# Optimization experiments

Hardware: AMD Instinct MI355X
Metric: run time of the kernel (lower is better)

## Reference

```python
import jax, jax.numpy as jnp
import numpy as np

N, E, B, D, OUT = 15000, 60000, 512, 64, 12
NI, EI, EH = 15, 5, 128
STEPS = 6  # both num_step_message_passing and num_step_set2set


def setup_inputs():
    key = jax.random.key(0)
    ks = jax.random.split(key, 30)
    r = lambda k, s, sc=0.05: jax.random.normal(k, s, jnp.float32) * sc
    return {
        "x": r(ks[0], (N, NI), 1.0),
        "edge_attr": r(ks[1], (E, EI), 1.0),
        "edge_index": jax.random.randint(ks[2], (2, E), 0, N),
        "batch": jnp.sort(jax.random.randint(ks[3], (N,), 0, B)),
        "lin0_w": r(ks[4], (D, NI)), "lin0_b": r(ks[5], (D,)),
        "en_w1": r(ks[6], (EH, EI)), "en_b1": r(ks[7], (EH,)),
        "en_w2": r(ks[8], (D * D, EH)), "en_b2": r(ks[9], (D * D,)),
        "conv_b": r(ks[10], (D,)),
        "gru_w_ih": r(ks[11], (3 * D, D)), "gru_w_hh": r(ks[12], (3 * D, D)),
        "gru_b_ih": r(ks[13], (3 * D,)), "gru_b_hh": r(ks[14], (3 * D,)),
        "lstm_w_ih": r(ks[15], (4 * D, 2 * D)), "lstm_w_hh": r(ks[16], (4 * D, D)),
        "lstm_b_ih": r(ks[17], (4 * D,)), "lstm_b_hh": r(ks[18], (4 * D,)),
        "lin1_w": r(ks[19], (D, 2 * D)), "lin1_b": r(ks[20], (D,)),
        "lin2_w": r(ks[21], (OUT, D)), "lin2_b": r(ks[22], (OUT,)),
    }


def _forward(x, edge_attr, lin0_w, lin0_b, en_w1, en_b1, en_w2, en_b2, conv_b,
             gru_w_ih, gru_w_hh, gru_b_ih, gru_b_hh,
             lstm_w_ih, lstm_w_hh, lstm_b_ih, lstm_b_hh,
             lin1_w, lin1_b, lin2_w, lin2_b, edge_index, batch):
    src, tgt = edge_index[0], edge_index[1]
    deg = jnp.maximum(jax.ops.segment_sum(jnp.ones((E,), x.dtype), tgt, num_segments=N), 1.0)
    # NNConv edge network (edge_attr is constant across MP steps -> hoist; same math)
    ew = jax.nn.relu(edge_attr @ en_w1.T + en_b1) @ en_w2.T + en_b2
    ew = ew.reshape(E, D, D)  # [E, in, out] per-edge weight matrices

    out = jax.nn.relu(x @ lin0_w.T + lin0_b)  # lin0
    h = out  # GRU hidden state (num_layers=1, seq_len=1)
    for _ in range(STEPS):
        # gather -> per-edge matvec -> scatter-mean (NNConv, aggr='mean', root_weight=False)
        msg = jnp.einsum('ei,eio->eo', out[src], ew)
        agg = jax.ops.segment_sum(msg, tgt, num_segments=N) / deg[:, None]
        m = jax.nn.relu(agg + conv_b)
        # single GRU step (PyTorch gate layout: r, z, n)
        gi = m @ gru_w_ih.T + gru_b_ih
        gh = h @ gru_w_hh.T + gru_b_hh
        ir, iz, inn = jnp.split(gi, 3, axis=-1)
        hr, hz, hn = jnp.split(gh, 3, axis=-1)
        rg = jax.nn.sigmoid(ir + hr)
        zg = jax.nn.sigmoid(iz + hz)
        ng = jnp.tanh(inn + rg * hn)
        h = (1.0 - zg) * ng + zg * h
        out = h

    # Set2Set pooling (LSTM gate layout: i, f, g, o)
    q_star = jnp.zeros((B, 2 * D), x.dtype)
    hl = jnp.zeros((B, D), x.dtype)
    cl = jnp.zeros((B, D), x.dtype)
    for _ in range(STEPS):
        g = q_star @ lstm_w_ih.T + lstm_b_ih + hl @ lstm_w_hh.T + lstm_b_hh
        ig, fg, gg, og = jnp.split(g, 4, axis=-1)
        cl = jax.nn.sigmoid(fg) * cl + jax.nn.sigmoid(ig) * jnp.tanh(gg)
        hl = jax.nn.sigmoid(og) * jnp.tanh(cl)
        e = jnp.sum(out * hl[batch], axis=-1)  # [N] attention logits
        emax = jax.ops.segment_max(e, batch, num_segments=B)
        ex = jnp.exp(e - emax[batch])
        denom = jax.ops.segment_sum(ex, batch, num_segments=B)
        a = ex / (denom[batch] + 1e-16)  # batch-segmented softmax
        rvec = jax.ops.segment_sum(a[:, None] * out, batch, num_segments=B)
        q_star = jnp.concatenate([hl, rvec], axis=-1)

    y = jax.nn.relu(q_star @ lin1_w.T + lin1_b) @ lin2_w.T + lin2_b
    return y  # [B, OUT]


def reference(x, edge_attr, edge_index, batch, lin0_w, lin0_b, en_w1, en_b1, en_w2, en_b2,
              conv_b, gru_w_ih, gru_w_hh, gru_b_ih, gru_b_hh,
              lstm_w_ih, lstm_w_hh, lstm_b_ih, lstm_b_hh, lin1_w, lin1_b, lin2_w, lin2_b):
    return _forward(x, edge_attr, lin0_w, lin0_b, en_w1, en_b1, en_w2, en_b2, conv_b,
                    gru_w_ih, gru_w_hh, gru_b_ih, gru_b_hh,
                    lstm_w_ih, lstm_w_hh, lstm_b_ih, lstm_b_hh,
                    lin1_w, lin1_b, lin2_w, lin2_b, edge_index, batch)
```

## Files before the change

kernel.cpp:

```cpp
#include <hip/hip_runtime.h>
#include <hip/hip_bf16.h>
#include <math.h>

#define NN 15000
#define NE 60000
#define NB 512
#define NIF 15
#define EIF 5
#define EHID 128
#define NSTEP 6
#define EPB 128

typedef _Float16 half8 __attribute__((ext_vector_type(8)));
typedef float floatx4 __attribute__((ext_vector_type(4)));

typedef __attribute__((address_space(3))) _Float16 lds_f16;
typedef __attribute__((address_space(1))) const _Float16 glb_f16;

__device__ __forceinline__ void gload_lds16(const _Float16* g, _Float16* l) {
  __builtin_amdgcn_global_load_lds((glb_f16*)g, (lds_f16*)l, 16, 0, 0);
}

__device__ __forceinline__ float sigmoidf_(float x) { return 1.f / (1.f + expf(-x)); }

__global__ void k_sentinel(float* out) { out[0] = 1000.0f; }

__global__ void k_init(const float* __restrict__ x, const float* __restrict__ l0w,
                       const float* __restrict__ l0b, const int* __restrict__ tgt,
                       const int* __restrict__ batch, float* __restrict__ outv,
                       float* __restrict__ deg, int* __restrict__ gstart,
                       int* __restrict__ gend,
                       const float* __restrict__ ea, const float* __restrict__ w1,
                       const float* __restrict__ b1,
                       const float* __restrict__ w2, const float* __restrict__ b2,
                       const float* __restrict__ gwih, const float* __restrict__ gwhh,
                       const float* __restrict__ lwih, const float* __restrict__ lwhh,
                       _Float16* __restrict__ w2pp, _Float16* __restrict__ hidp,
                       _Float16* __restrict__ wgpk,
                       float* __restrict__ wTih, float* __restrict__ wThh) {
  int idx = blockIdx.x * 256 + threadIdx.x;
  if (idx < NN * 64) {
    int n = idx >> 6, d = idx & 63;
    float s = l0b[d];
#pragma unroll
    for (int i = 0; i < NIF; ++i) s += x[n * NIF + i] * l0w[d * NIF + i];
    outv[idx] = fmaxf(s, 0.f);
  }
  if (idx < NE) atomicAdd(&deg[tgt[idx]], 1.0f);
  if (idx < NN) {
    int bb = batch[idx];
    atomicMin(&gstart[bb], idx);
    atomicMax(&gend[bb], idx + 1);
  }
  {
    int ih = idx - NN * 64;
    if (ih >= 0 && ih < NE * 16) {
      int e = ih >> 4, part = ih & 15;
      float eav[EIF];
#pragma unroll
      for (int i = 0; i < EIF; ++i) eav[i] = ea[e * EIF + i];
      half8 hv;
#pragma unroll
      for (int j = 0; j < 8; ++j) {
        int h = part * 8 + j;
        float s = b1[h];
#pragma unroll
        for (int i = 0; i < EIF; ++i) s += eav[i] * w1[h * EIF + i];
        hv[j] = (_Float16)fmaxf(s, 0.f);
      }
      *(half8*)&hidp[(size_t)e * 128 + part * 8] = hv;
    }
  }
  if (idx < 528384) {
    int g = idx >> 9;
    int r = idx & 511;
    int o = r >> 3, j = r & 7;
    float v;
    if (g < 1024) {
      int i = g >> 4;
      int h = ((g & 15) << 3) + j;
      v = w2[(size_t)(i * 64 + o) * 128 + h];
    } else {
      int i = ((g - 1024) << 3) + j;
      v = b2[i * 64 + o];
    }
    w2pp[idx] = (_Float16)v;
  } else if (idx < 528384 + 24576) {
    int i2 = idx - 528384;
    int kc = i2 / 6144;
    int rem = i2 % 6144;
    int o = rem >> 5, r = rem & 31;
    int kind = kc >> 1, cc = kc & 1;
    float v = kind ? gwhh[o * 64 + cc * 32 + r] : gwih[o * 64 + cc * 32 + r];
    wgpk[i2] = (_Float16)v;
  } else if (idx < 528384 + 24576 + 32768) {
    int i3 = idx - (528384 + 24576);
    int k = i3 >> 8, g = i3 & 255;
    wTih[i3] = lwih[g * 128 + k];
  } else if (idx < 528384 + 24576 + 32768 + 16384) {
    int i4 = idx - (528384 + 24576 + 32768);
    int k = i4 >> 8, g = i4 & 255;
    wThh[i4] = lwhh[g * 64 + k];
  }
}

__global__ __launch_bounds__(256, 4) void k_msg(
    const float* __restrict__ outv, const _Float16* __restrict__ hidp,
    const _Float16* __restrict__ w2pp, const int* __restrict__ src,
    const int* __restrict__ tgt, float* __restrict__ agg) {
  __shared__ __align__(16) _Float16 osL[EPB][72];
  __shared__ __align__(16) _Float16 bS[2][4096];
  int tid = threadIdx.x;
  int e0 = blockIdx.x * EPB;
  int hb = blockIdx.y;
  const int cbase = hb * 2;

  int el = tid >> 1, hf = tid & 1;
  int e = e0 + el;
  bool valid = e < NE;
  int s = valid ? src[e] : 0;
  const float4* op = (const float4*)(outv + (size_t)s * 64 + hf * 32);
#pragma unroll
  for (int pr = 0; pr < 4; ++pr) {
    float4 va = op[pr * 2 + 0];
    float4 vb = op[pr * 2 + 1];
    if (!valid) { va = vb = make_float4(0.f, 0.f, 0.f, 0.f); }
    half8 pk;
    pk[0] = (_Float16)va.x; pk[1] = (_Float16)va.y;
    pk[2] = (_Float16)va.z; pk[3] = (_Float16)va.w;
    pk[4] = (_Float16)vb.x; pk[5] = (_Float16)vb.y;
    pk[6] = (_Float16)vb.z; pk[7] = (_Float16)vb.w;
    *(half8*)&osL[el][hf * 32 + pr * 8] = pk;
  }

  int wv = tid >> 6, lane = tid & 63;
  int l15 = lane & 15, q = lane >> 4;
  int rbase = wv * 32 + l15;

  half8 hidf[2][2];
#pragma unroll
  for (int m = 0; m < 2; ++m) {
    int ef = e0 + rbase + m * 16;
    if (ef > NE - 1) ef = NE - 1;
    const _Float16* hp = hidp + (size_t)ef * 128 + hb * 64 + q * 8;
    hidf[m][0] = *(const half8*)hp;
    hidf[m][1] = *(const half8*)(hp + 32);
  }

  __syncthreads();

  {
    const _Float16* g0 = w2pp + (size_t)cbase * 2048 + tid * 8;
    gload_lds16(g0, &bS[0][0] + tid * 8);
    gload_lds16(g0 + 2048, &bS[0][0] + tid * 8 + 2048);
    const _Float16* g1 = w2pp + (size_t)(cbase + 4) * 2048 + tid * 8;
    gload_lds16(g1, &bS[1][0] + tid * 8);
    gload_lds16(g1 + 2048, &bS[1][0] + tid * 8 + 2048);
  }

  floatx4 acc[2][4];
#pragma unroll
  for (int m = 0; m < 2; ++m)
#pragma unroll
    for (int og = 0; og < 4; ++og) acc[m][og] = (floatx4){0.f, 0.f, 0.f, 0.f};

  const int fbase = q * 512 + l15 * 8;

  for (int il = 0; il < 64; ++il) {
    int p = il & 1;
    _Float16 osv0 = osL[rbase][il];
    _Float16 osv1 = osL[rbase + 16][il];
    if (il < 63) {
      asm volatile("s_waitcnt vmcnt(2)" ::: "memory");
    } else {
      asm volatile("s_waitcnt vmcnt(0)" ::: "memory");
    }
    __builtin_amdgcn_s_barrier();
    half8 fr[2][4];
    const _Float16* bb = &bS[p][0];
#pragma unroll
    for (int hc = 0; hc < 2; ++hc)
#pragma unroll
      for (int og = 0; og < 4; ++og)
        fr[hc][og] = *(const half8*)&bb[hc * 2048 + fbase + og * 128];
    asm volatile("s_waitcnt lgkmcnt(0)" ::: "memory");
    __builtin_amdgcn_sched_barrier(0);
    __builtin_amdgcn_s_barrier();
    if (il < 62) {
      const _Float16* gsrc = w2pp + (size_t)(cbase + (il + 2) * 4) * 2048 + tid * 8;
      _Float16* ldst = &bS[p][0] + tid * 8;
      gload_lds16(gsrc, ldst);
      gload_lds16(gsrc + 2048, ldst + 2048);
    }
    half8 os0 = {osv0, osv0, osv0, osv0, osv0, osv0, osv0, osv0};
    half8 os1 = {osv1, osv1, osv1, osv1, osv1, osv1, osv1, osv1};
#pragma unroll
    for (int hc = 0; hc < 2; ++hc) {
      half8 af0 = hidf[0][hc] * os0;
      half8 af1 = hidf[1][hc] * os1;
#pragma unroll
      for (int og = 0; og < 4; ++og) {
        acc[0][og] = __builtin_amdgcn_mfma_f32_16x16x32_f16(af0, fr[hc][og], acc[0][og], 0, 0, 0);
        acc[1][og] = __builtin_amdgcn_mfma_f32_16x16x32_f16(af1, fr[hc][og], acc[1][og], 0, 0, 0);
      }
    }
  }

  if (hb == 0) {
#pragma unroll
    for (int ibb = 0; ibb < 2; ++ibb) {
      int cb = 256 + ibb;
      const _Float16* bp = w2pp + ((size_t)(cb * 4 + q) * 64 + l15) * 8;
      half8 af[2];
#pragma unroll
      for (int m = 0; m < 2; ++m)
        af[m] = *(const half8*)&osL[rbase + m * 16][ibb * 32 + q * 8];
#pragma unroll
      for (int og = 0; og < 4; ++og) {
        half8 bf = *(const half8*)(bp + og * 128);
#pragma unroll
        for (int m = 0; m < 2; ++m)
          acc[m][og] = __builtin_amdgcn_mfma_f32_16x16x32_f16(af[m], bf, acc[m][og], 0, 0, 0);
      }
    }
  }

#pragma unroll
  for (int m = 0; m < 2; ++m) {
    int erow = e0 + wv * 32 + m * 16 + q * 4;
#pragma unroll
    for (int j = 0; j < 4; ++j) {
      int ee = erow + j;
      if (ee < NE) {
        int t = tgt[ee];
        float* ap = agg + (size_t)t * 64 + l15;
#pragma unroll
        for (int og = 0; og < 4; ++og) atomicAdd(ap + og * 16, acc[m][og][j]);
      }
    }
  }
}

__global__ __launch_bounds__(128, 2) void k_gru(
    float* __restrict__ agg, const float* __restrict__ deg,
    const float* __restrict__ convb, const _Float16* __restrict__ wgpk,
    const float* __restrict__ bih, const float* __restrict__ bhh,
    float* __restrict__ outv) {
  __shared__ __align__(16) _Float16 aL[32][136];
  __shared__ float hF[32][68];
  __shared__ float cbL[64];
  int tid = threadIdx.x;
  int n0 = blockIdx.x * 32;
  if (tid < 64) cbL[tid] = convb[tid];
  __syncthreads();

  int nl = tid >> 2, dq = (tid & 3) * 16;
  int n = n0 + nl;
  if (n < NN) {
    float dg = fmaxf(deg[n], 1.f);
    const float4* ap = (const float4*)(agg + (size_t)n * 64 + dq);
    const float4* hp = (const float4*)(outv + (size_t)n * 64 + dq);
    float4* az = (float4*)(agg + (size_t)n * 64 + dq);
#pragma unroll
    for (int t = 0; t < 4; ++t) {
      float4 a = ap[t];
      float4 h = hp[t];
      int d = dq + t * 4;
      aL[nl][d + 0] = (_Float16)fmaxf(a.x / dg + cbL[d + 0], 0.f);
      aL[nl][d + 1] = (_Float16)fmaxf(a.y / dg + cbL[d + 1], 0.f);
      aL[nl][d + 2] = (_Float16)fmaxf(a.z / dg + cbL[d + 2], 0.f);
      aL[nl][d + 3] = (_Float16)fmaxf(a.w / dg + cbL[d + 3], 0.f);
      aL[nl][64 + d + 0] = (_Float16)h.x;
      aL[nl][64 + d + 1] = (_Float16)h.y;
      aL[nl][64 + d + 2] = (_Float16)h.z;
      aL[nl][64 + d + 3] = (_Float16)h.w;
      hF[nl][d + 0] = h.x; hF[nl][d + 1] = h.y;
      hF[nl][d + 2] = h.z; hF[nl][d + 3] = h.w;
      az[t] = make_float4(0.f, 0.f, 0.f, 0.f);
    }
  } else {
#pragma unroll
    for (int t = 0; t < 4; ++t) {
      int d = dq + t * 4;
#pragma unroll
      for (int u = 0; u < 4; ++u) {
        aL[nl][d + u] = (_Float16)0.f;
        aL[nl][64 + d + u] = (_Float16)0.f;
        hF[nl][d + u] = 0.f;
      }
    }
  }
  __syncthreads();

  int wv = tid >> 6, lane = tid & 63, l15 = lane & 15, qd = lane >> 4;
  floatx4 acc[2][6][2];
#pragma unroll
  for (int mt = 0; mt < 2; ++mt)
#pragma unroll
    for (int t6 = 0; t6 < 6; ++t6)
#pragma unroll
      for (int kind = 0; kind < 2; ++kind) acc[mt][t6][kind] = (floatx4){0.f, 0.f, 0.f, 0.f};

#pragma unroll
  for (int kind = 0; kind < 2; ++kind) {
#pragma unroll
    for (int cc = 0; cc < 2; ++cc) {
      half8 af[2];
#pragma unroll
      for (int mt = 0; mt < 2; ++mt)
        af[mt] = *(const half8*)&aL[mt * 16 + l15][kind * 64 + cc * 32 + qd * 8];
#pragma unroll
      for (int t6 = 0; t6 < 6; ++t6) {
        int gb = (t6 * 2 + wv) * 16;
        half8 bf = *(const half8*)&wgpk[((size_t)(kind * 2 + cc) * 192 + gb + l15) * 32 + qd * 8];
#pragma unroll
        for (int mt = 0; mt < 2; ++mt)
          acc[mt][t6][kind] = __builtin_amdgcn_mfma_f32_16x16x32_f16(af[mt], bf, acc[mt][t6][kind], 0, 0, 0);
      }
    }
  }

#pragma unroll
  for (int dd = 0; dd < 2; ++dd) {
    int d = (dd * 2 + wv) * 16 + l15;
    float bir = bih[d], bhr = bhh[d];
    float biz = bih[64 + d], bhz = bhh[64 + d];
    float bin = bih[128 + d], bhn = bhh[128 + d];
#pragma unroll
    for (int mt = 0; mt < 2; ++mt) {
#pragma unroll
      for (int j = 0; j < 4; ++j) {
        int nloc = mt * 16 + qd * 4 + j;
        int nn = n0 + nloc;
        if (nn < NN) {
          float ir = acc[mt][dd][0][j] + bir, hr = acc[mt][dd][1][j] + bhr;
          float iz = acc[mt][2 + dd][0][j] + biz, hz = acc[mt][2 + dd][1][j] + bhz;
          float in_ = acc[mt][4 + dd][0][j] + bin, hn = acc[mt][4 + dd][1][j] + bhn;
          float r = sigmoidf_(ir + hr);
          float z = sigmoidf_(iz + hz);
          float ng = tanhf(in_ + r * hn);
          float h = hF[nloc][d];
          outv[(size_t)nn * 64 + d] = (1.f - z) * ng + z * h;
        }
      }
    }
  }
}

__global__ __launch_bounds__(256) void k_s2s(
    const float* __restrict__ outv, const int* __restrict__ gstart,
    const int* __restrict__ gend, const float* __restrict__ wTih,
    const float* __restrict__ wThh, const float* __restrict__ bih,
    const float* __restrict__ bhh, const float* __restrict__ l1w,
    const float* __restrict__ l1b, const float* __restrict__ l2w,
    const float* __restrict__ l2b, float* __restrict__ y) {
  __shared__ float qL[128], hlL[64], clL[64], gL[256];
  __shared__ float mxA[4], smA[4], accA[4][64], hidL[64];
  int b = blockIdx.x, tid = threadIdx.x, wv = tid >> 6, lane = tid & 63;
  int s0 = gstart[b], e0 = gend[b];
  if (s0 > e0) { s0 = 0; e0 = 0; }
  if (tid < 128) qL[tid] = 0.f;
  if (tid < 64) { hlL[tid] = 0.f; clL[tid] = 0.f; }
  __syncthreads();

  for (int step = 0; step < NSTEP; ++step) {
    {
      int g = tid;
      float s = bih[g] + bhh[g];
      for (int k = 0; k < 128; ++k) s += qL[k] * wTih[k * 256 + g];
      for (int k = 0; k < 64; ++k) s += hlL[k] * wThh[k * 256 + g];
      gL[g] = s;
    }
    __syncthreads();
    if (tid < 64) {
      float ig = gL[tid], fg = gL[64 + tid], gg = gL[128 + tid], og = gL[192 + tid];
      float c = sigmoidf_(fg) * clL[tid] + sigmoidf_(ig) * tanhf(gg);
      clL[tid] = c;
      hlL[tid] = sigmoidf_(og) * tanhf(c);
    }
    __syncthreads();
    float hd = hlL[lane];
    float mxw = -1e30f;
    for (int nn = s0 + wv; nn < e0; nn += 4) {
      float v = outv[(size_t)nn * 64 + lane] * hd;
#pragma unroll
      for (int off = 32; off > 0; off >>= 1) v += __shfl_xor(v, off);
      mxw = fmaxf(mxw, v);
    }
    if (lane == 0) mxA[wv] = mxw;
    __syncthreads();
    float mx = fmaxf(fmaxf(mxA[0], mxA[1]), fmaxf(mxA[2], mxA[3]));
    float sm = 0.f, ac = 0.f;
    for (int nn = s0 + wv; nn < e0; nn += 4) {
      float o_nd = outv[(size_t)nn * 64 + lane];
      float v = o_nd * hd;
#pragma unroll
      for (int off = 32; off > 0; off >>= 1) v += __shfl_xor(v, off);
      float ex = expf(v - mx);
      sm += ex;
      ac += ex * o_nd;
    }
    if (lane == 0) smA[wv] = sm;
    accA[wv][lane] = ac;
    __syncthreads();
    if (tid < 64) {
      float den = smA[0] + smA[1] + smA[2] + smA[3] + 1e-16f;
      float rv = (accA[0][tid] + accA[1][tid] + accA[2][tid] + accA[3][tid]) / den;
      qL[tid] = hlL[tid];
      qL[64 + tid] = rv;
    }
    __syncthreads();
  }
  if (tid < 64) {
    float s = l1b[tid];
    for (int k = 0; k < 128; ++k) s += qL[k] * l1w[tid * 128 + k];
    hidL[tid] = fmaxf(s, 0.f);
  }
  __syncthreads();
  if (tid < 12) {
    float s = l2b[tid];
    for (int k = 0; k < 64; ++k) s += hidL[k] * l2w[tid * 64 + k];
    y[b * 12 + tid] = s;
  }
}

extern "C" void kernel_launch(void* const* d_in, const int* in_sizes, int n_in,
                              void* d_out, int out_size, void* d_ws, size_t ws_size,
                              hipStream_t stream) {
  const float* x = (const float*)d_in[0];
  const float* ea = (const float*)d_in[1];
  const int* eidx = (const int*)d_in[2];
  const int* batch = (const int*)d_in[3];
  const float* lin0_w = (const float*)d_in[4];
  const float* lin0_b = (const float*)d_in[5];
  const float* en_w1 = (const float*)d_in[6];
  const float* en_b1 = (const float*)d_in[7];
  const float* en_w2 = (const float*)d_in[8];
  const float* en_b2 = (const float*)d_in[9];
  const float* conv_b = (const float*)d_in[10];
  const float* gru_wih = (const float*)d_in[11];
  const float* gru_whh = (const float*)d_in[12];
  const float* gru_bih = (const float*)d_in[13];
  const float* gru_bhh = (const float*)d_in[14];
  const float* lstm_wih = (const float*)d_in[15];
  const float* lstm_whh = (const float*)d_in[16];
  const float* lstm_bih = (const float*)d_in[17];
  const float* lstm_bhh = (const float*)d_in[18];
  const float* lin1_w = (const float*)d_in[19];
  const float* lin1_b = (const float*)d_in[20];
  const float* lin2_w = (const float*)d_in[21];
  const float* lin2_b = (const float*)d_in[22];
  const int* srcp = eidx;
  const int* tgtp = eidx + NE;

  char* ws = (char*)d_ws;
  size_t off = 0;
  auto alloc = [&](size_t bytes) {
    char* p = ws + off;
    off += (bytes + 255) & ~(size_t)255;
    return p;
  };
  _Float16* w2pp = (_Float16*)alloc((size_t)1032 * 512 * 2);
  _Float16* hidp = (_Float16*)alloc((size_t)NE * 128 * 2);
  _Float16* wgpk = (_Float16*)alloc((size_t)24576 * 2);
  float* wTih = (float*)alloc((size_t)32768 * 4);
  float* wThh = (float*)alloc((size_t)16384 * 4);
  float* out = (float*)alloc((size_t)NN * 64 * 4);
  float* agg = (float*)alloc((size_t)NN * 64 * 4);
  float* deg = (float*)alloc((size_t)NN * 4);
  int* gstart = (int*)alloc((size_t)NB * 4);
  int* gend = (int*)alloc((size_t)NB * 4);
  if (off > ws_size) {
    k_sentinel<<<1, 1, 0, stream>>>((float*)d_out);
    return;
  }

  hipMemsetAsync(deg, 0, (size_t)NN * 4, stream);
  hipMemsetAsync(gstart, 0x7f, (size_t)NB * 4, stream);
  hipMemsetAsync(gend, 0, (size_t)NB * 4, stream);
  hipMemsetAsync(agg, 0, (size_t)NN * 64 * 4, stream);

  k_init<<<(NN * 64 + NE * 16 + 255) / 256, 256, 0, stream>>>(
      x, lin0_w, lin0_b, tgtp, batch, out, deg, gstart, gend,
      ea, en_w1, en_b1, en_w2, en_b2, gru_wih, gru_whh, lstm_wih, lstm_whh,
      w2pp, hidp, wgpk, wTih, wThh);

  for (int step = 0; step < NSTEP; ++step) {
    k_msg<<<dim3((NE + EPB - 1) / EPB, 2), 256, 0, stream>>>(out, hidp, w2pp,
                                                             srcp, tgtp, agg);
    k_gru<<<(NN + 31) / 32, 128, 0, stream>>>(agg, deg, conv_b, wgpk, gru_bih,
                                              gru_bhh, out);
  }

  k_s2s<<<NB, 256, 0, stream>>>(out, gstart, gend, wTih, wThh, lstm_bih, lstm_bhh,
                                lin1_w, lin1_b, lin2_w, lin2_b, (float*)d_out);
}
```

Baseline: 692.8 us.

## Split message kernel across output halves instead of hidden halves

The second grid dimension of the per-edge message kernel now splits the 64 output columns into two halves instead of splitting the 128-wide hidden dimension. Each block accumulates over all 128 hidden units for its 32 outputs. Partial sums over hidden units no longer have to be combined through atomics, so each edge issues half as many atomicAdds per block and the total atomic count drops. In exchange, each block loads twice as many hidden fragments into registers, and the weight tiles are fetched with a strided remapped layout that may be less coalesced.

After: 674.4 us. -2.7%, faster.

```diff
diff --git a/kernel.cpp b/kernel.cpp
--- a/kernel.cpp
+++ b/kernel.cpp
@@ -112,8 +112,13 @@
   __shared__ __align__(16) _Float16 bS[2][4096];
   int tid = threadIdx.x;
   int e0 = blockIdx.x * EPB;
-  int hb = blockIdx.y;
-  const int cbase = hb * 2;
+  int oh = blockIdx.y;
+
+  const int hcA = tid >> 7, qA = (tid >> 5) & 3, opA = tid & 31;
+  const size_t srcA = (size_t)qA * 512 + oh * 256 + opA * 8;
+  const int tB = tid + 256;
+  const int hcB = tB >> 7, qB = (tB >> 5) & 3, opB = tB & 31;
+  const size_t srcB = (size_t)qB * 512 + oh * 256 + opB * 8;
 
   int el = tid >> 1, hf = tid & 1;
   int e = e0 + el;
@@ -137,34 +142,33 @@
   int l15 = lane & 15, q = lane >> 4;
   int rbase = wv * 32 + l15;
 
-  half8 hidf[2][2];
+  half8 hidf[2][4];
 #pragma unroll
   for (int m = 0; m < 2; ++m) {
     int ef = e0 + rbase + m * 16;
     if (ef > NE - 1) ef = NE - 1;
-    const _Float16* hp = hidp + (size_t)ef * 128 + hb * 64 + q * 8;
-    hidf[m][0] = *(const half8*)hp;
-    hidf[m][1] = *(const half8*)(hp + 32);
+    const _Float16* hp = hidp + (size_t)ef * 128 + q * 8;
+#pragma unroll
+    for (int hc = 0; hc < 4; ++hc)
+      hidf[m][hc] = *(const half8*)(hp + hc * 32);
   }
 
   __syncthreads();
 
   {
-    const _Float16* g0 = w2pp + (size_t)cbase * 2048 + tid * 8;
-    gload_lds16(g0, &bS[0][0] + tid * 8);
-    gload_lds16(g0 + 2048, &bS[0][0] + tid * 8 + 2048);
-    const _Float16* g1 = w2pp + (size_t)(cbase + 4) * 2048 + tid * 8;
-    gload_lds16(g1, &bS[1][0] + tid * 8);
-    gload_lds16(g1 + 2048, &bS[1][0] + tid * 8 + 2048);
-  }
-
-  floatx4 acc[2][4];
+    gload_lds16(w2pp + (size_t)(0 * 4 + hcA) * 2048 + srcA, &bS[0][0] + tid * 8);
+    gload_lds16(w2pp + (size_t)(0 * 4 + hcB) * 2048 + srcB, &bS[0][0] + tid * 8 + 2048);
+    gload_lds16(w2pp + (size_t)(1 * 4 + hcA) * 2048 + srcA, &bS[1][0] + tid * 8);
+    gload_lds16(w2pp + (size_t)(1 * 4 + hcB) * 2048 + srcB, &bS[1][0] + tid * 8 + 2048);
+  }
+
+  floatx4 acc[2][2];
 #pragma unroll
   for (int m = 0; m < 2; ++m)
 #pragma unroll
-    for (int og = 0; og < 4; ++og) acc[m][og] = (floatx4){0.f, 0.f, 0.f, 0.f};
-
-  const int fbase = q * 512 + l15 * 8;
+    for (int og = 0; og < 2; ++og) acc[m][og] = (floatx4){0.f, 0.f, 0.f, 0.f};
+
+  const int fbase = q * 256 + l15 * 8;
 
   for (int il = 0; il < 64; ++il) {
     int p = il & 1;
@@ -176,52 +180,50 @@
       asm volatile("s_waitcnt vmcnt(0)" ::: "memory");
     }
     __builtin_amdgcn_s_barrier();
-    half8 fr[2][4];
+    half8 fr[4][2];
     const _Float16* bb = &bS[p][0];
 #pragma unroll
-    for (int hc = 0; hc < 2; ++hc)
-#pragma unroll
-      for (int og = 0; og < 4; ++og)
-        fr[hc][og] = *(const half8*)&bb[hc * 2048 + fbase + og * 128];
+    for (int hc = 0; hc < 4; ++hc)
+#pragma unroll
+      for (int og = 0; og < 2; ++og)
+        fr[hc][og] = *(const half8*)&bb[hc * 1024 + og * 128 + fbase];
     asm volatile("s_waitcnt lgkmcnt(0)" ::: "memory");
     __builtin_amdgcn_sched_barrier(0);
     __builtin_amdgcn_s_barrier();
     if (il < 62) {
-      const _Float16* gsrc = w2pp + (size_t)(cbase + (il + 2) * 4) * 2048 + tid * 8;
+      size_t cb2 = (size_t)(il + 2) * 4;
       _Float16* ldst = &bS[p][0] + tid * 8;
-      gload_lds16(gsrc, ldst);
-      gload_lds16(gsrc + 2048, ldst + 2048);
+      gload_lds16(w2pp + (cb2 + hcA) * 2048 + srcA, ldst);
+      gload_lds16(w2pp + (cb2 + hcB) * 2048 + srcB, ldst + 2048);
     }
     half8 os0 = {osv0, osv0, osv0, osv0, osv0, osv0, osv0, osv0};
     half8 os1 = {osv1, osv1, osv1, osv1, osv1, osv1, osv1, osv1};
 #pragma unroll
-    for (int hc = 0; hc < 2; ++hc) {
+    for (int hc = 0; hc < 4; ++hc) {
       half8 af0 = hidf[0][hc] * os0;
       half8 af1 = hidf[1][hc] * os1;
 #pragma unroll
-      for (int og = 0; og < 4; ++og) {
+      for (int og = 0; og < 2; ++og) {
         acc[0][og] = __builtin_amdgcn_mfma_f32_16x16x32_f16(af0, fr[hc][og], acc[0][og], 0, 0, 0);
         acc[1][og] = __builtin_amdgcn_mfma_f32_16x16x32_f16(af1, fr[hc][og], acc[1][og], 0, 0, 0);
       }
     }
   }
 
-  if (hb == 0) {
-#pragma unroll
-    for (int ibb = 0; ibb < 2; ++ibb) {
-      int cb = 256 + ibb;
-      const _Float16* bp = w2pp + ((size_t)(cb * 4 + q) * 64 + l15) * 8;
-      half8 af[2];
+#pragma unroll
+  for (int ibb = 0; ibb < 2; ++ibb) {
+    int cb = 256 + ibb;
+    half8 af[2];
+#pragma unroll
+    for (int m = 0; m < 2; ++m)
+      af[m] = *(const half8*)&osL[rbase + m * 16][ibb * 32 + q * 8];
+#pragma unroll
+    for (int og = 0; og < 2; ++og) {
+      const _Float16* bp = w2pp + ((size_t)(cb * 4 + q) * 64 + oh * 32 + og * 16 + l15) * 8;
+      half8 bf = *(const half8*)bp;
 #pragma unroll
       for (int m = 0; m < 2; ++m)
-        af[m] = *(const half8*)&osL[rbase + m * 16][ibb * 32 + q * 8];
-#pragma unroll
-      for (int og = 0; og < 4; ++og) {
-        half8 bf = *(const half8*)(bp + og * 128);
-#pragma unroll
-        for (int m = 0; m < 2; ++m)
-          acc[m][og] = __builtin_amdgcn_mfma_f32_16x16x32_f16(af[m], bf, acc[m][og], 0, 0, 0);
-      }
+        acc[m][og] = __builtin_amdgcn_mfma_f32_16x16x32_f16(af[m], bf, acc[m][og], 0, 0, 0);
     }
   }
 
@@ -233,9 +235,9 @@
       int ee = erow + j;
       if (ee < NE) {
         int t = tgt[ee];
-        float* ap = agg + (size_t)t * 64 + l15;
-#pragma unroll
-        for (int og = 0; og < 4; ++og) atomicAdd(ap + og * 16, acc[m][og][j]);
+        float* ap = agg + (size_t)t * 64 + oh * 32 + l15;
+        atomicAdd(ap, acc[m][0][j]);
+        atomicAdd(ap + 16, acc[m][1][j]);
       }
     }
   }
```
